# Optimization experiments

Hardware: AMD Instinct MI355X
Metric: run time of the kernel (lower is better)

## Reference

```python
import jax, jax.numpy as jnp
import numpy as np

B = 131072          # points on manifold
A = 16              # n_anchors
SDIM = 512          # substrate.n (spatial dim); ambient dim = SDIM + 1
ALPHA = 0.1         # attraction coefficient
EPS = 1e-7


def _proj(p):
    # Project onto hyperboloid: recompute time coord from spatial part.
    sp = p[..., 1:]
    t = jnp.sqrt(1.0 + jnp.sum(sp * sp, axis=-1, keepdims=True))
    return jnp.concatenate([t, sp], axis=-1)


def _linner(x, y):
    # Lorentz inner product <x,y>_L = -x0*y0 + sum_i xi*yi
    return -x[..., 0] * y[..., 0] + jnp.sum(x[..., 1:] * y[..., 1:], axis=-1)


def setup_inputs() -> dict:
    key = jax.random.key(0)
    k1, k2 = jax.random.split(key)
    x_sp = jax.random.normal(k1, (B, SDIM), dtype=jnp.float32)
    x = _proj(jnp.concatenate([jnp.zeros((B, 1), jnp.float32), x_sp], axis=-1))
    a_sp = jax.random.normal(k2, (A, SDIM), dtype=jnp.float32) * 0.01
    anchors = _proj(jnp.concatenate([jnp.zeros((A, 1), jnp.float32), a_sp], axis=-1))
    return {"x": x, "anchors": anchors}


def reference(x, anchors):
    af = _proj(anchors)                                   # [A, D]
    D = af.shape[-1]
    metric = jnp.concatenate([-jnp.ones((1,), x.dtype), jnp.ones((D - 1,), x.dtype)])
    # pairwise -<x,a>_L  -> [B, A]
    theta_all = -jnp.einsum('bd,ad->ba', x * metric, af)
    dists = jnp.arccosh(jnp.clip(theta_all, 1.0 + EPS, None))
    idx = jnp.argmin(dists, axis=1)                       # nearest anchor per point
    y = af[idx]                                           # [B, D]
    # log_map_x(y) = acosh(theta)/sqrt(theta^2-1) * (y - theta*x)
    theta = jnp.clip(-_linner(x, y), 1.0 + EPS, None)[:, None]
    direction = (jnp.arccosh(theta) / jnp.sqrt(theta * theta - 1.0)) * (y - theta * x)
    v = ALPHA * direction                                 # tangent vector
    # exp_map_x(v) = cosh(||v||_L) x + sinh(||v||_L)/||v||_L * v
    vn = jnp.sqrt(jnp.clip(_linner(v, v), EPS, None))[:, None]
    return jnp.cosh(vn) * x + (jnp.sinh(vn) / vn) * v
```

## Files before the change

kernel.cpp:

```cpp
#include <hip/hip_runtime.h>

#define NA 16
#define DD 513
#define ALPHA 0.1f
#define EPSV 1e-7f
#define GRID 2048

typedef __fp16 h2v __attribute__((ext_vector_type(2)));
typedef __fp16 f16x8 __attribute__((ext_vector_type(8)));
typedef float f32x4 __attribute__((ext_vector_type(4)));
typedef unsigned int u32;

union H2U { h2v h; u32 u; };
union FU  { float f; u32 u; int i; };
union FRAG { u32 w[4]; f16x8 v; };
union U4   { uint4 v; u32 w[4]; };

static __device__ __forceinline__ u32 pkrtz(float lo, float hi) {
    H2U t; t.h = __builtin_amdgcn_cvt_pkrtz(lo, hi); return t.u;
}
static __device__ __forceinline__ h2v asH2(u32 w) { H2U t; t.u = w; return t.h; }

static __device__ __forceinline__ int swz(int G) {
    return G ^ (((G >> 4) & 3) | (((G >> 6) & 1) << 2));
}

__global__ __launch_bounds__(256, 2)
void hfield_kernel(const float* __restrict__ x,
                   const float* __restrict__ anc,
                   float* __restrict__ out) {
    __shared__ uint4 bframe[1024];
    __shared__ uint4 xframe[4][1024];

    const int tid = threadIdx.x, lane = tid & 63, wid = tid >> 6;
    const int col = lane & 15, g = lane >> 4;

#pragma unroll
    for (int m = 0; m < 4; ++m) {
        const int F = m * 256 + tid;
        const int l = F & 63, kt = F >> 6;
        const int a = l & 15, lp = 4 * kt + (l >> 4);
        const float* p = anc + a * DD + 1 + lp;
        uint4 w;
        w.x = pkrtz(p[0],   p[64]);
        w.y = pkrtz(p[128], p[192]);
        w.z = pkrtz(p[256], p[320]);
        w.w = pkrtz(p[384], p[448]);
        bframe[swz(F)] = w;
    }

    float af0c;
    {
        const float* p = anc + col * DD + 1 + g * 128;
        float s = 0.f;
#pragma unroll 16
        for (int i = 0; i < 128; ++i) s = fmaf(p[i], p[i], s);
        s += __shfl_xor(s, 16);
        s += __shfl_xor(s, 32);
        af0c = sqrtf(1.0f + s);
    }
    __syncthreads();

    const int rowbase = (blockIdx.x * 4 + wid) * 16;
    uint4* xf = xframe[wid];
    const float* xb = x + (size_t)rowbase * DD;

    float x0r[4];
#pragma unroll
    for (int r4 = 0; r4 < 4; ++r4) x0r[r4] = xb[(size_t)(4 * g + r4) * DD];

#pragma unroll 8
    for (int r = 0; r < 16; ++r) {
        const float* p = xb + (size_t)r * DD + 1 + lane;
        float v[8];
#pragma unroll
        for (int j = 0; j < 8; ++j) v[j] = p[64 * j];
        uint4 w;
        w.x = pkrtz(v[0], v[1]);
        w.y = pkrtz(v[2], v[3]);
        w.z = pkrtz(v[4], v[5]);
        w.w = pkrtz(v[6], v[7]);
        xf[swz((lane >> 2) * 64 + 16 * (lane & 3) + r)] = w;
    }
    asm volatile("s_waitcnt lgkmcnt(0)" ::: "memory");

    f32x4 acc = {0.f, 0.f, 0.f, 0.f};
#pragma unroll
    for (int kt = 0; kt < 16; ++kt) {
        FRAG A, B;
        U4 ax, bx;
        ax.v = xf[swz(kt * 64 + lane)];
        bx.v = bframe[swz(kt * 64 + lane)];
        A.w[0] = ax.w[0]; A.w[1] = ax.w[1]; A.w[2] = ax.w[2]; A.w[3] = ax.w[3];
        B.w[0] = bx.w[0]; B.w[1] = bx.w[1]; B.w[2] = bx.w[2]; B.w[3] = bx.w[3];
        acc = __builtin_amdgcn_mfma_f32_16x16x32_f16(A.v, B.v, acc, 0, 0, 0);
    }

    const float thmin = 1.0f + 1e-7f;
    float c1r[4], c2r[4], o0r[4];
    int bir[4];
#pragma unroll
    for (int r4 = 0; r4 < 4; ++r4) {
        const float th = fmaxf(fmaf(x0r[r4], af0c, -acc[r4]), thmin);
        FU u; u.f = th;
        u32 key = (u.u & 0xFFFFFFF0u) | (u32)col;
#pragma unroll
        for (int m = 1; m <= 8; m <<= 1) {
            const u32 o = (u32)__shfl_xor((int)key, m);
            key = o < key ? o : key;
        }
        const int bi  = (int)(key & 15u);
        const int src = (lane & 48) | bi;
        const float thw = __shfl(th, src);
        const float y0  = __shfl(af0c, src);

        const float s2 = thw * thw - 1.0f;
        const float rr = sqrtf(s2);
        const float ac = __logf(thw + rr);
        const float cf = ac / rr;
        const float vn = sqrtf(fmaxf(ALPHA * ALPHA * ac * ac, EPSV));
        const float e  = __expf(vn);
        const float ei = 1.0f / e;
        const float ch = 0.5f * (e + ei);
        const float sh = 0.5f * (e - ei);
        const float c2 = ALPHA * cf * (sh / vn);
        const float c1 = fmaf(-c2, thw, ch);

        c1r[r4] = c1;
        c2r[r4] = c2;
        o0r[r4] = fmaf(c2, y0, c1 * x0r[r4]);
        bir[r4] = bi;
    }

#pragma unroll 4
    for (int r = 0; r < 16; ++r) {
        const int src = (r >> 2) * 16;
        const float c1 = __shfl(c1r[r & 3], src);
        const float c2 = __shfl(c2r[r & 3], src);
        const float o0 = __shfl(o0r[r & 3], src);
        const int   bi = __builtin_amdgcn_readfirstlane(__shfl(bir[r & 3], src));

        U4 X, Y;
        X.v = xf[swz((lane >> 2) * 64 + 16 * (lane & 3) + r)];
        Y.v = bframe[swz((lane >> 2) * 64 + 16 * (lane & 3) + bi)];

        float* op = out + (size_t)(rowbase + r) * DD;
        if (lane == 0) __builtin_nontemporal_store(o0, op);
#pragma unroll
        for (int q = 0; q < 4; ++q) {
            const h2v hx = asH2(X.w[q]);
            const h2v hy = asH2(Y.w[q]);
            __builtin_nontemporal_store(fmaf(c2, (float)hy.x, c1 * (float)hx.x),
                                        &op[1 + lane + 128 * q]);
            __builtin_nontemporal_store(fmaf(c2, (float)hy.y, c1 * (float)hx.y),
                                        &op[1 + lane + 64 + 128 * q]);
        }
    }
}

extern "C" void kernel_launch(void* const* d_in, const int* in_sizes, int n_in,
                              void* d_out, int out_size, void* d_ws, size_t ws_size,
                              hipStream_t stream) {
    const float* x   = (const float*)d_in[0];
    const float* anc = (const float*)d_in[1];
    float* out       = (float*)d_out;
    hipLaunchKernelGGL(hfield_kernel, dim3(GRID), dim3(256), 0, stream, x, anc, out);
}
```

Baseline: 112.1 us.

## Switch inner-product MFMA to fp8 and keep x halves in registers

Quantizes both x and the anchors (scaled by 16) to fp8 in shared memory and uses the 16x16x32 fp8 MFMA in place of the f16 one, which halves LDS footprint and traffic. The fp16 copy of x is now held in registers across rows for the output pass, and the anchor row for the output is read back from fp8. Launch bounds go to 4 blocks per CU. Both argmin and the output's anchor term now use fp8 precision, which risks picking the wrong anchor and adding output error. The extra registers may also conflict with the higher occupancy target and cause spills.

```diff
diff --git a/kernel.cpp b/kernel.cpp
--- a/kernel.cpp
+++ b/kernel.cpp
@@ -7,46 +7,41 @@
 #define GRID 2048
 
 typedef __fp16 h2v __attribute__((ext_vector_type(2)));
-typedef __fp16 f16x8 __attribute__((ext_vector_type(8)));
+typedef float f32x2 __attribute__((ext_vector_type(2)));
 typedef float f32x4 __attribute__((ext_vector_type(4)));
 typedef unsigned int u32;
+typedef unsigned long long u64;
 
 union H2U { h2v h; u32 u; };
 union FU  { float f; u32 u; int i; };
-union FRAG { u32 w[4]; f16x8 v; };
-union U4   { uint4 v; u32 w[4]; };
 
 static __device__ __forceinline__ u32 pkrtz(float lo, float hi) {
     H2U t; t.h = __builtin_amdgcn_cvt_pkrtz(lo, hi); return t.u;
 }
 static __device__ __forceinline__ h2v asH2(u32 w) { H2U t; t.u = w; return t.h; }
 
-static __device__ __forceinline__ int swz(int G) {
-    return G ^ (((G >> 4) & 3) | (((G >> 6) & 1) << 2));
+static __device__ __forceinline__ int swz(int row, int a) {
+    return row * 128 + (a ^ ((row & 15) << 1));
 }
 
-__global__ __launch_bounds__(256, 2)
+__global__ __launch_bounds__(256, 4)
 void hfield_kernel(const float* __restrict__ x,
                    const float* __restrict__ anc,
                    float* __restrict__ out) {
-    __shared__ uint4 bframe[1024];
-    __shared__ uint4 xframe[4][1024];
+    __shared__ u32 bframe[NA * 128];
+    __shared__ u32 xframe[4][16 * 128];
 
     const int tid = threadIdx.x, lane = tid & 63, wid = tid >> 6;
     const int col = lane & 15, g = lane >> 4;
 
 #pragma unroll
-    for (int m = 0; m < 4; ++m) {
-        const int F = m * 256 + tid;
-        const int l = F & 63, kt = F >> 6;
-        const int a = l & 15, lp = 4 * kt + (l >> 4);
-        const float* p = anc + a * DD + 1 + lp;
-        uint4 w;
-        w.x = pkrtz(p[0],   p[64]);
-        w.y = pkrtz(p[128], p[192]);
-        w.z = pkrtz(p[256], p[320]);
-        w.w = pkrtz(p[384], p[448]);
-        bframe[swz(F)] = w;
+    for (int m = 0; m < 8; ++m) {
+        const int i = m * 256 + tid;
+        const int ar = i >> 7, a = i & 127, l = a >> 1, h = a & 1;
+        const float* p = anc + ar * DD + 1 + l + 256 * h;
+        int w = __builtin_amdgcn_cvt_pk_fp8_f32(p[0] * 16.f, p[64] * 16.f, 0, false);
+        w = __builtin_amdgcn_cvt_pk_fp8_f32(p[128] * 16.f, p[192] * 16.f, w, true);
+        bframe[swz(ar, a)] = (u32)w;
     }
 
     float af0c;
@@ -62,38 +57,37 @@
     __syncthreads();
 
     const int rowbase = (blockIdx.x * 4 + wid) * 16;
-    uint4* xf = xframe[wid];
+    u32* xf = xframe[wid];
     const float* xb = x + (size_t)rowbase * DD;
 
     float x0r[4];
 #pragma unroll
     for (int r4 = 0; r4 < 4; ++r4) x0r[r4] = xb[(size_t)(4 * g + r4) * DD];
 
-#pragma unroll 8
+    u32 xq[16][4];
+#pragma unroll
     for (int r = 0; r < 16; ++r) {
         const float* p = xb + (size_t)r * DD + 1 + lane;
         float v[8];
 #pragma unroll
         for (int j = 0; j < 8; ++j) v[j] = p[64 * j];
-        uint4 w;
-        w.x = pkrtz(v[0], v[1]);
-        w.y = pkrtz(v[2], v[3]);
-        w.z = pkrtz(v[4], v[5]);
-        w.w = pkrtz(v[6], v[7]);
-        xf[swz((lane >> 2) * 64 + 16 * (lane & 3) + r)] = w;
+#pragma unroll
+        for (int m = 0; m < 4; ++m) xq[r][m] = pkrtz(v[2 * m], v[2 * m + 1]);
+        int qa = __builtin_amdgcn_cvt_pk_fp8_f32(v[0], v[1], 0, false);
+        qa = __builtin_amdgcn_cvt_pk_fp8_f32(v[2], v[3], qa, true);
+        int qb = __builtin_amdgcn_cvt_pk_fp8_f32(v[4], v[5], 0, false);
+        qb = __builtin_amdgcn_cvt_pk_fp8_f32(v[6], v[7], qb, true);
+        *reinterpret_cast<uint2*>(&xf[swz(r, 2 * lane)]) = make_uint2((u32)qa, (u32)qb);
     }
     asm volatile("s_waitcnt lgkmcnt(0)" ::: "memory");
 
     f32x4 acc = {0.f, 0.f, 0.f, 0.f};
 #pragma unroll
     for (int kt = 0; kt < 16; ++kt) {
-        FRAG A, B;
-        U4 ax, bx;
-        ax.v = xf[swz(kt * 64 + lane)];
-        bx.v = bframe[swz(kt * 64 + lane)];
-        A.w[0] = ax.w[0]; A.w[1] = ax.w[1]; A.w[2] = ax.w[2]; A.w[3] = ax.w[3];
-        B.w[0] = bx.w[0]; B.w[1] = bx.w[1]; B.w[2] = bx.w[2]; B.w[3] = bx.w[3];
-        acc = __builtin_amdgcn_mfma_f32_16x16x32_f16(A.v, B.v, acc, 0, 0, 0);
+        const int fi = swz(col, 8 * kt + 2 * g);
+        const u64 A = *reinterpret_cast<const u64*>(&xf[fi]);
+        const u64 B = *reinterpret_cast<const u64*>(&bframe[fi]);
+        acc = __builtin_amdgcn_mfma_f32_16x16x32_fp8_fp8((long)A, (long)B, acc, 0, 0, 0);
     }
 
     const float thmin = 1.0f + 1e-7f;
@@ -101,7 +95,7 @@
     int bir[4];
 #pragma unroll
     for (int r4 = 0; r4 < 4; ++r4) {
-        const float th = fmaxf(fmaf(x0r[r4], af0c, -acc[r4]), thmin);
+        const float th = fmaxf(fmaf(x0r[r4], af0c, -acc[r4] * 0.0625f), thmin);
         FU u; u.f = th;
         u32 key = (u.u & 0xFFFFFFF0u) | (u32)col;
 #pragma unroll
@@ -132,28 +126,34 @@
         bir[r4] = bi;
     }
 
-#pragma unroll 4
+#pragma unroll
     for (int r = 0; r < 16; ++r) {
         const int src = (r >> 2) * 16;
-        const float c1 = __shfl(c1r[r & 3], src);
-        const float c2 = __shfl(c2r[r & 3], src);
-        const float o0 = __shfl(o0r[r & 3], src);
-        const int   bi = __builtin_amdgcn_readfirstlane(__shfl(bir[r & 3], src));
+        const float c1  = __shfl(c1r[r & 3], src);
+        const float c2  = __shfl(c2r[r & 3], src);
+        const float o0  = __shfl(o0r[r & 3], src);
+        const int   bi  = __builtin_amdgcn_readfirstlane(__shfl(bir[r & 3], src));
+        const float c2s = c2 * 0.0625f;
 
-        U4 X, Y;
-        X.v = xf[swz((lane >> 2) * 64 + 16 * (lane & 3) + r)];
-        Y.v = bframe[swz((lane >> 2) * 64 + 16 * (lane & 3) + bi)];
+        const uint2 yq = *reinterpret_cast<const uint2*>(&bframe[swz(bi, 2 * lane)]);
+        float yv[8];
+        { f32x2 t = __builtin_amdgcn_cvt_pk_f32_fp8((int)yq.x, false); yv[0] = t.x; yv[1] = t.y; }
+        { f32x2 t = __builtin_amdgcn_cvt_pk_f32_fp8((int)yq.x, true);  yv[2] = t.x; yv[3] = t.y; }
+        { f32x2 t = __builtin_amdgcn_cvt_pk_f32_fp8((int)yq.y, false); yv[4] = t.x; yv[5] = t.y; }
+        { f32x2 t = __builtin_amdgcn_cvt_pk_f32_fp8((int)yq.y, true);  yv[6] = t.x; yv[7] = t.y; }
+        float ysl[8];
+        ysl[0] = yv[0]; ysl[1] = yv[1]; ysl[2] = yv[2]; ysl[3] = yv[3];
+        ysl[4] = yv[4]; ysl[5] = yv[5]; ysl[6] = yv[6]; ysl[7] = yv[7];
 
         float* op = out + (size_t)(rowbase + r) * DD;
         if (lane == 0) __builtin_nontemporal_store(o0, op);
 #pragma unroll
-        for (int q = 0; q < 4; ++q) {
-            const h2v hx = asH2(X.w[q]);
-            const h2v hy = asH2(Y.w[q]);
-            __builtin_nontemporal_store(fmaf(c2, (float)hy.x, c1 * (float)hx.x),
-                                        &op[1 + lane + 128 * q]);
-            __builtin_nontemporal_store(fmaf(c2, (float)hy.y, c1 * (float)hx.y),
-                                        &op[1 + lane + 64 + 128 * q]);
+        for (int m = 0; m < 4; ++m) {
+            const h2v hx = asH2(xq[r][m]);
+            __builtin_nontemporal_store(fmaf(c2s, ysl[2 * m],     c1 * (float)hx.x),
+                                        &op[1 + lane + 64 * (2 * m)]);
+            __builtin_nontemporal_store(fmaf(c2s, ysl[2 * m + 1], c1 * (float)hx.y),
+                                        &op[1 + lane + 64 * (2 * m + 1)]);
         }
     }
 }
```

Result: slower. 155.0 us (+38.3%).

## Share one 16-row tile per block across four waves with redundant MFMA

Applied to the files above, without the earlier changes.

Each block now handles 16 rows instead of 64. Its four waves each load and pack 4 rows into a single shared x tile, then all four waves run the same 16x16 MFMA over the whole tile and each writes out its own 4 rows. This cuts LDS per block, allowing higher occupancy (launch bounds raised to 5 blocks per SM) and a 4x larger grid, aiming to hide global memory latency better. In exchange, the MFMA and epilogue math are computed redundantly by all four waves, the anchor frame is repacked 4x more often across the grid, and a block-wide barrier is added.

```diff
diff --git a/kernel.cpp b/kernel.cpp
--- a/kernel.cpp
+++ b/kernel.cpp
@@ -4,7 +4,7 @@
 #define DD 513
 #define ALPHA 0.1f
 #define EPSV 1e-7f
-#define GRID 2048
+#define GRID 8192
 
 typedef __fp16 h2v __attribute__((ext_vector_type(2)));
 typedef __fp16 f16x8 __attribute__((ext_vector_type(8)));
@@ -25,12 +25,12 @@
     return G ^ (((G >> 4) & 3) | (((G >> 6) & 1) << 2));
 }
 
-__global__ __launch_bounds__(256, 2)
+__global__ __launch_bounds__(256, 5)
 void hfield_kernel(const float* __restrict__ x,
                    const float* __restrict__ anc,
                    float* __restrict__ out) {
     __shared__ uint4 bframe[1024];
-    __shared__ uint4 xframe[4][1024];
+    __shared__ uint4 xframe[1024];
 
     const int tid = threadIdx.x, lane = tid & 63, wid = tid >> 6;
     const int col = lane & 15, g = lane >> 4;
@@ -59,18 +59,17 @@
         s += __shfl_xor(s, 32);
         af0c = sqrtf(1.0f + s);
     }
-    __syncthreads();
 
-    const int rowbase = (blockIdx.x * 4 + wid) * 16;
-    uint4* xf = xframe[wid];
+    const int rowbase = blockIdx.x * 16;
     const float* xb = x + (size_t)rowbase * DD;
 
     float x0r[4];
 #pragma unroll
     for (int r4 = 0; r4 < 4; ++r4) x0r[r4] = xb[(size_t)(4 * g + r4) * DD];
 
-#pragma unroll 8
-    for (int r = 0; r < 16; ++r) {
+#pragma unroll
+    for (int rr = 0; rr < 4; ++rr) {
+        const int r = 4 * wid + rr;
         const float* p = xb + (size_t)r * DD + 1 + lane;
         float v[8];
 #pragma unroll
@@ -80,16 +79,16 @@
         w.y = pkrtz(v[2], v[3]);
         w.z = pkrtz(v[4], v[5]);
         w.w = pkrtz(v[6], v[7]);
-        xf[swz((lane >> 2) * 64 + 16 * (lane & 3) + r)] = w;
+        xframe[swz((lane >> 2) * 64 + 16 * (lane & 3) + r)] = w;
     }
-    asm volatile("s_waitcnt lgkmcnt(0)" ::: "memory");
+    __syncthreads();
 
     f32x4 acc = {0.f, 0.f, 0.f, 0.f};
 #pragma unroll
     for (int kt = 0; kt < 16; ++kt) {
         FRAG A, B;
         U4 ax, bx;
-        ax.v = xf[swz(kt * 64 + lane)];
+        ax.v = xframe[swz(kt * 64 + lane)];
         bx.v = bframe[swz(kt * 64 + lane)];
         A.w[0] = ax.w[0]; A.w[1] = ax.w[1]; A.w[2] = ax.w[2]; A.w[3] = ax.w[3];
         B.w[0] = bx.w[0]; B.w[1] = bx.w[1]; B.w[2] = bx.w[2]; B.w[3] = bx.w[3];
@@ -132,16 +131,17 @@
         bir[r4] = bi;
     }
 
-#pragma unroll 4
-    for (int r = 0; r < 16; ++r) {
-        const int src = (r >> 2) * 16;
-        const float c1 = __shfl(c1r[r & 3], src);
-        const float c2 = __shfl(c2r[r & 3], src);
-        const float o0 = __shfl(o0r[r & 3], src);
-        const int   bi = __builtin_amdgcn_readfirstlane(__shfl(bir[r & 3], src));
+#pragma unroll
+    for (int rr = 0; rr < 4; ++rr) {
+        const int r   = 4 * wid + rr;
+        const int src = 16 * wid;
+        const float c1 = __shfl(c1r[rr], src);
+        const float c2 = __shfl(c2r[rr], src);
+        const float o0 = __shfl(o0r[rr], src);
+        const int   bi = __builtin_amdgcn_readfirstlane(__shfl(bir[rr], src));
 
         U4 X, Y;
-        X.v = xf[swz((lane >> 2) * 64 + 16 * (lane & 3) + r)];
+        X.v = xframe[swz((lane >> 2) * 64 + 16 * (lane & 3) + r)];
         Y.v = bframe[swz((lane >> 2) * 64 + 16 * (lane & 3) + bi)];
 
         float* op = out + (size_t)(rowbase + r) * DD;
```

After: 199.0 us. +77.5%, slower.

## Process two row tiles per wave with register prefetch of next tile

Applied to the files above, without the earlier changes.

Each wave now handles two 16-row tiles, which halves the grid. The first tile's x data is loaded into registers before the anchor setup so the load overlaps that work, and the second tile is prefetched into registers while the first is computed and stored. The aim is to hide global load latency and to spread the per-block anchor setup over more rows. In exchange, holding 128 floats per lane in registers raises register pressure and may lower occupancy below the launch-bounds target.

```diff
diff --git a/kernel.cpp b/kernel.cpp
--- a/kernel.cpp
+++ b/kernel.cpp
@@ -4,7 +4,8 @@
 #define DD 513
 #define ALPHA 0.1f
 #define EPSV 1e-7f
-#define GRID 2048
+#define TPW 2
+#define GRID 1024
 
 typedef __fp16 h2v __attribute__((ext_vector_type(2)));
 typedef __fp16 f16x8 __attribute__((ext_vector_type(8)));
@@ -35,6 +36,25 @@
     const int tid = threadIdx.x, lane = tid & 63, wid = tid >> 6;
     const int col = lane & 15, g = lane >> 4;
 
+    const int rowbase0 = (blockIdx.x * 4 + wid) * (16 * TPW);
+    const float* xb = x + (size_t)rowbase0 * DD;
+    uint4* xf = xframe[wid];
+
+    float nv[16][8];
+#pragma unroll
+    for (int r = 0; r < 16; ++r) {
+        const float* p = xb + (size_t)r * DD + 1 + lane;
+#pragma unroll
+        for (int j = 0; j < 8; ++j) nv[r][j] = p[64 * j];
+    }
+    float x0r[TPW][4];
+#pragma unroll
+    for (int t = 0; t < TPW; ++t)
+#pragma unroll
+        for (int r4 = 0; r4 < 4; ++r4)
+            x0r[t][r4] = xb[(size_t)(t * 16 + 4 * g + r4) * DD];
+    __builtin_amdgcn_sched_barrier(0);
+
 #pragma unroll
     for (int m = 0; m < 4; ++m) {
         const int F = m * 256 + tid;
@@ -61,99 +81,107 @@
     }
     __syncthreads();
 
-    const int rowbase = (blockIdx.x * 4 + wid) * 16;
-    uint4* xf = xframe[wid];
-    const float* xb = x + (size_t)rowbase * DD;
+    const float thmin = 1.0f + 1e-7f;
 
-    float x0r[4];
 #pragma unroll
-    for (int r4 = 0; r4 < 4; ++r4) x0r[r4] = xb[(size_t)(4 * g + r4) * DD];
+    for (int t = 0; t < TPW; ++t) {
+        const int rowbase = rowbase0 + t * 16;
 
-#pragma unroll 8
-    for (int r = 0; r < 16; ++r) {
-        const float* p = xb + (size_t)r * DD + 1 + lane;
-        float v[8];
+        if (t > 0)
+            asm volatile("s_waitcnt lgkmcnt(0)" ::: "memory");
 #pragma unroll
-        for (int j = 0; j < 8; ++j) v[j] = p[64 * j];
-        uint4 w;
-        w.x = pkrtz(v[0], v[1]);
-        w.y = pkrtz(v[2], v[3]);
-        w.z = pkrtz(v[4], v[5]);
-        w.w = pkrtz(v[6], v[7]);
-        xf[swz((lane >> 2) * 64 + 16 * (lane & 3) + r)] = w;
-    }
-    asm volatile("s_waitcnt lgkmcnt(0)" ::: "memory");
+        for (int r = 0; r < 16; ++r) {
+            uint4 w;
+            w.x = pkrtz(nv[r][0], nv[r][1]);
+            w.y = pkrtz(nv[r][2], nv[r][3]);
+            w.z = pkrtz(nv[r][4], nv[r][5]);
+            w.w = pkrtz(nv[r][6], nv[r][7]);
+            xf[swz((lane >> 2) * 64 + 16 * (lane & 3) + r)] = w;
+        }
 
-    f32x4 acc = {0.f, 0.f, 0.f, 0.f};
+        if (t + 1 < TPW) {
+            const float* nb = xb + (size_t)((t + 1) * 16) * DD;
 #pragma unroll
-    for (int kt = 0; kt < 16; ++kt) {
-        FRAG A, B;
-        U4 ax, bx;
-        ax.v = xf[swz(kt * 64 + lane)];
-        bx.v = bframe[swz(kt * 64 + lane)];
-        A.w[0] = ax.w[0]; A.w[1] = ax.w[1]; A.w[2] = ax.w[2]; A.w[3] = ax.w[3];
-        B.w[0] = bx.w[0]; B.w[1] = bx.w[1]; B.w[2] = bx.w[2]; B.w[3] = bx.w[3];
-        acc = __builtin_amdgcn_mfma_f32_16x16x32_f16(A.v, B.v, acc, 0, 0, 0);
-    }
+            for (int r = 0; r < 16; ++r) {
+                const float* p = nb + (size_t)r * DD + 1 + lane;
+#pragma unroll
+                for (int j = 0; j < 8; ++j) nv[r][j] = p[64 * j];
+            }
+            __builtin_amdgcn_sched_barrier(0);
+        }
 
-    const float thmin = 1.0f + 1e-7f;
-    float c1r[4], c2r[4], o0r[4];
-    int bir[4];
+        asm volatile("s_waitcnt lgkmcnt(0)" ::: "memory");
+
+        f32x4 acc = {0.f, 0.f, 0.f, 0.f};
 #pragma unroll
-    for (int r4 = 0; r4 < 4; ++r4) {
-        const float th = fmaxf(fmaf(x0r[r4], af0c, -acc[r4]), thmin);
-        FU u; u.f = th;
-        u32 key = (u.u & 0xFFFFFFF0u) | (u32)col;
+        for (int kt = 0; kt < 16; ++kt) {
+            FRAG A, B;
+            U4 ax, bx;
+            ax.v = xf[swz(kt * 64 + lane)];
+            bx.v = bframe[swz(kt * 64 + lane)];
+            A.w[0] = ax.w[0]; A.w[1] = ax.w[1]; A.w[2] = ax.w[2]; A.w[3] = ax.w[3];
+            B.w[0] = bx.w[0]; B.w[1] = bx.w[1]; B.w[2] = bx.w[2]; B.w[3] = bx.w[3];
+            acc = __builtin_amdgcn_mfma_f32_16x16x32_f16(A.v, B.v, acc, 0, 0, 0);
+        }
+
+        float c1r[4], c2r[4], o0r[4];
+        int bir[4];
 #pragma unroll
-        for (int m = 1; m <= 8; m <<= 1) {
-            const u32 o = (u32)__shfl_xor((int)key, m);
-            key = o < key ? o : key;
+        for (int r4 = 0; r4 < 4; ++r4) {
+            const float th = fmaxf(fmaf(x0r[t][r4], af0c, -acc[r4]), thmin);
+            FU u; u.f = th;
+            u32 key = (u.u & 0xFFFFFFF0u) | (u32)col;
+#pragma unroll
+            for (int m = 1; m <= 8; m <<= 1) {
+                const u32 o = (u32)__shfl_xor((int)key, m);
+                key = o < key ? o : key;
+            }
+            const int bi  = (int)(key & 15u);
+            const int src = (lane & 48) | bi;
+            const float thw = __shfl(th, src);
+            const float y0  = __shfl(af0c, src);
+
+            const float s2 = thw * thw - 1.0f;
+            const float rr = sqrtf(s2);
+            const float ac = __logf(thw + rr);
+            const float cf = ac / rr;
+            const float vn = sqrtf(fmaxf(ALPHA * ALPHA * ac * ac, EPSV));
+            const float e  = __expf(vn);
+            const float ei = 1.0f / e;
+            const float ch = 0.5f * (e + ei);
+            const float sh = 0.5f * (e - ei);
+            const float c2 = ALPHA * cf * (sh / vn);
+            const float c1 = fmaf(-c2, thw, ch);
+
+            c1r[r4] = c1;
+            c2r[r4] = c2;
+            o0r[r4] = fmaf(c2, y0, c1 * x0r[t][r4]);
+            bir[r4] = bi;
         }
-        const int bi  = (int)(key & 15u);
-        const int src = (lane & 48) | bi;
-        const float thw = __shfl(th, src);
-        const float y0  = __shfl(af0c, src);
-
-        const float s2 = thw * thw - 1.0f;
-        const float rr = sqrtf(s2);
-        const float ac = __logf(thw + rr);
-        const float cf = ac / rr;
-        const float vn = sqrtf(fmaxf(ALPHA * ALPHA * ac * ac, EPSV));
-        const float e  = __expf(vn);
-        const float ei = 1.0f / e;
-        const float ch = 0.5f * (e + ei);
-        const float sh = 0.5f * (e - ei);
-        const float c2 = ALPHA * cf * (sh / vn);
-        const float c1 = fmaf(-c2, thw, ch);
-
-        c1r[r4] = c1;
-        c2r[r4] = c2;
-        o0r[r4] = fmaf(c2, y0, c1 * x0r[r4]);
-        bir[r4] = bi;
-    }
 
 #pragma unroll 4
-    for (int r = 0; r < 16; ++r) {
-        const int src = (r >> 2) * 16;
-        const float c1 = __shfl(c1r[r & 3], src);
-        const float c2 = __shfl(c2r[r & 3], src);
-        const float o0 = __shfl(o0r[r & 3], src);
-        const int   bi = __builtin_amdgcn_readfirstlane(__shfl(bir[r & 3], src));
+        for (int r = 0; r < 16; ++r) {
+            const int src = (r >> 2) * 16;
+            const float c1 = __shfl(c1r[r & 3], src);
+            const float c2 = __shfl(c2r[r & 3], src);
+            const float o0 = __shfl(o0r[r & 3], src);
+            const int   bi = __builtin_amdgcn_readfirstlane(__shfl(bir[r & 3], src));
 
-        U4 X, Y;
-        X.v = xf[swz((lane >> 2) * 64 + 16 * (lane & 3) + r)];
-        Y.v = bframe[swz((lane >> 2) * 64 + 16 * (lane & 3) + bi)];
+            U4 X, Y;
+            X.v = xf[swz((lane >> 2) * 64 + 16 * (lane & 3) + r)];
+            Y.v = bframe[swz((lane >> 2) * 64 + 16 * (lane & 3) + bi)];
 
-        float* op = out + (size_t)(rowbase + r) * DD;
-        if (lane == 0) __builtin_nontemporal_store(o0, op);
+            float* op = out + (size_t)(rowbase + r) * DD;
+            if (lane == 0) __builtin_nontemporal_store(o0, op);
 #pragma unroll
-        for (int q = 0; q < 4; ++q) {
-            const h2v hx = asH2(X.w[q]);
-            const h2v hy = asH2(Y.w[q]);
-            __builtin_nontemporal_store(fmaf(c2, (float)hy.x, c1 * (float)hx.x),
-                                        &op[1 + lane + 128 * q]);
-            __builtin_nontemporal_store(fmaf(c2, (float)hy.y, c1 * (float)hx.y),
-                                        &op[1 + lane + 64 + 128 * q]);
+            for (int q = 0; q < 4; ++q) {
+                const h2v hx = asH2(X.w[q]);
+                const h2v hy = asH2(Y.w[q]);
+                __builtin_nontemporal_store(fmaf(c2, (float)hy.x, c1 * (float)hx.x),
+                                            &op[1 + lane + 128 * q]);
+                __builtin_nontemporal_store(fmaf(c2, (float)hy.y, c1 * (float)hx.y),
+                                            &op[1 + lane + 64 + 128 * q]);
+            }
         }
     }
 }
```

Result: no change. 111.1 us (-0.9%).
